# Optimization experiments

Hardware: AMD Instinct MI355X
Metric: run time of the kernel (lower is better)

## Reference

```python
import jax, jax.numpy as jnp
import numpy as np

N_CELL, N_TISSUE, H, NH = 200000, 2000, 256, 8
HD = H // NH
SCALE = HD ** -0.5
EPS = 1e-5


def _layernorm(x, g, b):
    m = jnp.mean(x, axis=-1, keepdims=True)
    v = jnp.mean((x - m) ** 2, axis=-1, keepdims=True)
    return (x - m) / jnp.sqrt(v + EPS) * g + b


def setup_inputs() -> dict:
    key = jax.random.key(0)
    ks = jax.random.split(key, 12)
    s = 0.02

    def lin(k):
        k1, k2 = jax.random.split(k)
        return (jax.random.normal(k1, (H, H), jnp.float32) * s,
                jax.random.normal(k2, (H,), jnp.float32) * s)

    Wq_bu, bq_bu = lin(ks[0])
    Wk_bu, bk_bu = lin(ks[1])
    Wv_bu, bv_bu = lin(ks[2])
    Wo_bu, bo_bu = lin(ks[3])
    Wv_td, bv_td = lin(ks[4])
    Wo_td, bo_td = lin(ks[5])
    return dict(
        cell_features=jax.random.normal(ks[6], (N_CELL, H), jnp.float32),
        tissue_features=jax.random.normal(ks[7], (N_TISSUE, H), jnp.float32),
        cluster_labels=jax.random.randint(ks[8], (N_CELL,), 0, N_TISSUE, dtype=jnp.int32),
        tissue_batch=jnp.zeros((N_TISSUE,), jnp.int32),
        Wq_bu=Wq_bu, bq_bu=bq_bu, Wk_bu=Wk_bu, bk_bu=bk_bu,
        Wv_bu=Wv_bu, bv_bu=bv_bu, Wo_bu=Wo_bu, bo_bu=bo_bu,
        Wv_td=Wv_td, bv_td=bv_td, Wo_td=Wo_td, bo_td=bo_td,
        ln_cell_g=jnp.ones((H,), jnp.float32), ln_cell_b=jnp.zeros((H,), jnp.float32),
        ln_tissue_g=jnp.ones((H,), jnp.float32), ln_tissue_b=jnp.zeros((H,), jnp.float32),
    )


def reference(cell_features, tissue_features, cluster_labels, tissue_batch,
              Wq_bu, bq_bu, Wk_bu, bk_bu, Wv_bu, bv_bu, Wo_bu, bo_bu,
              Wv_td, bv_td, Wo_td, bo_td,
              ln_cell_g, ln_cell_b, ln_tissue_g, ln_tissue_b):
    Nc = cell_features.shape[0]
    Nt = tissue_features.shape[0]

    # ---- bottom-up: each tissue node (1 query) attends over its cells (segment attention) ----
    Q = (tissue_features @ Wq_bu + bq_bu).reshape(Nt, NH, HD)   # [Nt, h, d]
    K = (cell_features @ Wk_bu + bk_bu).reshape(Nc, NH, HD)     # [Nc, h, d]
    V = (cell_features @ Wv_bu + bv_bu).reshape(Nc, NH, HD)     # [Nc, h, d]

    # per-cell score against its own cluster's tissue query
    scores = jnp.einsum('nhd,nhd->nh', K, Q[cluster_labels]) * SCALE  # [Nc, h]
    smax = jax.lax.stop_gradient(
        jax.ops.segment_max(scores, cluster_labels, num_segments=Nt))  # [Nt, h]
    ex = jnp.exp(scores - smax[cluster_labels])
    denom = jax.ops.segment_sum(ex, cluster_labels, num_segments=Nt)   # [Nt, h]
    w = ex / denom[cluster_labels]                                     # [Nc, h]
    attended = jax.ops.segment_sum(w[..., None] * V, cluster_labels,
                                   num_segments=Nt)                    # [Nt, h, d]
    attended = attended.reshape(Nt, H) @ Wo_bu + bo_bu

    counts = jax.ops.segment_sum(jnp.ones((Nc,), cell_features.dtype),
                                 cluster_labels, num_segments=Nt)
    tissue_updated = jnp.where(counts[:, None] > 0, attended, tissue_features)

    # ---- top-down: each cell attends to its single tissue token ----
    # softmax over a single key is identically 1, so q/k projections cancel:
    # attended_cell = out_proj(v_proj(tissue_updated[cluster]))
    td_per_tissue = (tissue_updated @ Wv_td + bv_td) @ Wo_td + bo_td   # [Nt, H]
    cell_updated = td_per_tissue[cluster_labels]                       # [Nc, H]

    cell_out = _layernorm(cell_features + cell_updated, ln_cell_g, ln_cell_b)
    tissue_out = _layernorm(tissue_features + tissue_updated, ln_tissue_g, ln_tissue_b)
    return (cell_out, tissue_out)
```

## Files before the change

### kernel.cpp

```cpp
#include <hip/hip_runtime.h>
#include <math.h>

#define NC 200000
#define NT 2000
#define HH 256
#define NH_ 8
#define SCALE 0.17677669529663687f
#define EPS 1e-5f


__global__ void k_hist(const int* __restrict__ labels, int* __restrict__ counts) {
  int i = blockIdx.x * 256 + threadIdx.x;
  if (i < NC) atomicAdd(&counts[labels[i]], 1);
}

__global__ void k_scan(const int* __restrict__ counts, int* __restrict__ offsets) {
  int tid = threadIdx.x;
  int base = tid * 32;
  int local[32];
  int s = 0;
  #pragma unroll
  for (int k = 0; k < 32; k++) {
    int idx = base + k;
    int v = (idx < NT) ? counts[idx] : 0;
    local[k] = s;
    s += v;
  }
  int incl = s;
  #pragma unroll
  for (int d = 1; d < 64; d <<= 1) {
    int o = __shfl_up(incl, d, 64);
    if (tid >= d) incl += o;
  }
  int excl = incl - s;
  #pragma unroll
  for (int k = 0; k < 32; k++) {
    int idx = base + k;
    if (idx < NT) offsets[idx] = excl + local[k];
  }
  if (tid == 63) offsets[NT] = incl;
}

__global__ void k_scatter(const int* __restrict__ labels, const int* __restrict__ offsets,
                          int* __restrict__ cursor, int* __restrict__ cindex) {
  int i = blockIdx.x * 256 + threadIdx.x;
  if (i < NC) {
    int c = labels[i];
    int pos = offsets[c] + atomicAdd(&cursor[c], 1);
    cindex[pos] = i;
  }
}


__global__ __launch_bounds__(256) void k_gemm_bias(
    const float* __restrict__ A, const float* __restrict__ W,
    const float* __restrict__ bias, float* __restrict__ C, int M)
{
  __shared__ float Al[16][33];
  __shared__ float Wl[32][HH];
  int tid = threadIdx.x;
  int r0 = blockIdx.x * 16;
  float acc[16];
  #pragma unroll
  for (int r = 0; r < 16; r++) acc[r] = 0.f;
  for (int k0 = 0; k0 < HH; k0 += 32) {
    for (int e = tid; e < 16 * 32; e += 256) {
      int r = e >> 5, k = e & 31;
      int row = r0 + r;
      Al[r][k] = (row < M) ? A[(size_t)row * HH + k0 + k] : 0.f;
    }
    for (int e = tid; e < 32 * HH; e += 256) {
      int k = e >> 8, j = e & 255;
      Wl[k][j] = W[(size_t)(k0 + k) * HH + j];
    }
    __syncthreads();
    for (int k = 0; k < 32; k++) {
      float w = Wl[k][tid];
      #pragma unroll
      for (int r = 0; r < 16; r++) acc[r] += Al[r][k] * w;
    }
    __syncthreads();
  }
  float bj = bias[tid];
  #pragma unroll
  for (int r = 0; r < 16; r++) {
    int row = r0 + r;
    if (row < M) C[(size_t)row * HH + tid] = acc[r] + bj;
  }
}


__global__ __launch_bounds__(256) void k_qproj(
    const float* __restrict__ Q, const float* __restrict__ Wk, float* __restrict__ Qproj)
{
  __shared__ float Al[64][33];
  __shared__ float Bl[32][257];
  int h = blockIdx.x & 7, tb = blockIdx.x >> 3;
  int t0 = tb * 64;
  int tid = threadIdx.x;
  for (int e = tid; e < 64 * 32; e += 256) {
    int r = e >> 5, d = e & 31;
    int t = t0 + r;
    Al[r][d] = (t < NT) ? Q[(size_t)t * HH + h * 32 + d] * SCALE : 0.f;
  }
  for (int e = tid; e < 256 * 32; e += 256) {
    int j = e >> 5, d = e & 31;
    Bl[d][j] = Wk[(size_t)j * HH + h * 32 + d];
  }
  __syncthreads();
  float acc[64];
  #pragma unroll
  for (int r = 0; r < 64; r++) acc[r] = 0.f;
  for (int d = 0; d < 32; d++) {
    float b = Bl[d][tid];
    #pragma unroll
    for (int r = 0; r < 64; r++) acc[r] += Al[r][d] * b;
  }
  for (int r = 0; r < 64; r++) {
    int t = t0 + r;
    if (t < NT) Qproj[((size_t)t * NH_ + h) * HH + tid] = acc[r];
  }
}

__global__ void k_bkq(const float* __restrict__ Q, const float* __restrict__ bk,
                      float* __restrict__ bkq) {
  int g = blockIdx.x * 256 + threadIdx.x;
  if (g < NT * NH_) {
    int t = g >> 3, h = g & 7;
    float s = 0.f;
    #pragma unroll
    for (int d = 0; d < 32; d++) s += bk[h * 32 + d] * Q[(size_t)t * HH + h * 32 + d];
    bkq[g] = s * SCALE;
  }
}


__global__ __launch_bounds__(256) void k_cellpass(
    const float* __restrict__ cell, const int* __restrict__ cindex,
    const int* __restrict__ offsets, const float* __restrict__ Qproj,
    const float* __restrict__ bkq, float* __restrict__ Cwn)
{
  int t = blockIdx.x;
  int n0 = offsets[t], n1 = offsets[t + 1];
  if (n1 == n0) return;
  int tid = threadIdx.x;
  int wave = tid >> 6, lane = tid & 63;

  float qp[NH_][4];
  #pragma unroll
  for (int h = 0; h < NH_; h++) {
    float4 v = *reinterpret_cast<const float4*>(&Qproj[((size_t)t * NH_ + h) * HH + lane * 4]);
    qp[h][0] = v.x; qp[h][1] = v.y; qp[h][2] = v.z; qp[h][3] = v.w;
  }
  float bq[NH_];
  #pragma unroll
  for (int h = 0; h < NH_; h++) bq[h] = bkq[t * NH_ + h];

  float m[NH_], dsum[NH_], cw[NH_][4];
  #pragma unroll
  for (int h = 0; h < NH_; h++) {
    m[h] = -1e30f; dsum[h] = 0.f;
    cw[h][0] = cw[h][1] = cw[h][2] = cw[h][3] = 0.f;
  }

  for (int i = n0 + wave; i < n1; i += 4) {
    int n = cindex[i];
    float4 x = *reinterpret_cast<const float4*>(&cell[(size_t)n * HH + lane * 4]);
    float p[NH_];
    #pragma unroll
    for (int h = 0; h < NH_; h++)
      p[h] = x.x * qp[h][0] + x.y * qp[h][1] + x.z * qp[h][2] + x.w * qp[h][3];
    #pragma unroll
    for (int d = 1; d < 64; d <<= 1) {
      #pragma unroll
      for (int h = 0; h < NH_; h++) p[h] += __shfl_xor(p[h], d, 64);
    }
    float s[NH_];
    bool need = false;
    #pragma unroll
    for (int h = 0; h < NH_; h++) { s[h] = p[h] + bq[h]; need = need || (s[h] > m[h]); }
    if (need) {
      #pragma unroll
      for (int h = 0; h < NH_; h++) {
        float mn = fmaxf(m[h], s[h]);
        float sc = __expf(m[h] - mn);
        m[h] = mn;
        dsum[h] *= sc;
        cw[h][0] *= sc; cw[h][1] *= sc; cw[h][2] *= sc; cw[h][3] *= sc;
      }
    }
    #pragma unroll
    for (int h = 0; h < NH_; h++) {
      float e = __expf(s[h] - m[h]);
      dsum[h] += e;
      cw[h][0] += e * x.x; cw[h][1] += e * x.y; cw[h][2] += e * x.z; cw[h][3] += e * x.w;
    }
  }

  __shared__ float mlds[4][NH_];
  __shared__ float dlds[4][NH_];
  __shared__ float cwlds[NH_][HH];
  if (lane == 0) {
    #pragma unroll
    for (int h = 0; h < NH_; h++) { mlds[wave][h] = m[h]; dlds[wave][h] = dsum[h]; }
  }
  __syncthreads();
  float sw[NH_], dtot[NH_];
  #pragma unroll
  for (int h = 0; h < NH_; h++) {
    float g = fmaxf(fmaxf(mlds[0][h], mlds[1][h]), fmaxf(mlds[2][h], mlds[3][h]));
    sw[h] = __expf(m[h] - g);
    dtot[h] = dlds[0][h] * __expf(mlds[0][h] - g) + dlds[1][h] * __expf(mlds[1][h] - g)
            + dlds[2][h] * __expf(mlds[2][h] - g) + dlds[3][h] * __expf(mlds[3][h] - g);
  }
  if (wave == 0) {
    #pragma unroll
    for (int h = 0; h < NH_; h++) {
      cwlds[h][lane * 4 + 0] = cw[h][0] * sw[h];
      cwlds[h][lane * 4 + 1] = cw[h][1] * sw[h];
      cwlds[h][lane * 4 + 2] = cw[h][2] * sw[h];
      cwlds[h][lane * 4 + 3] = cw[h][3] * sw[h];
    }
  }
  __syncthreads();
  #pragma unroll
  for (int w = 1; w < 4; w++) {
    if (wave == w) {
      #pragma unroll
      for (int h = 0; h < NH_; h++) {
        cwlds[h][lane * 4 + 0] += cw[h][0] * sw[h];
        cwlds[h][lane * 4 + 1] += cw[h][1] * sw[h];
        cwlds[h][lane * 4 + 2] += cw[h][2] * sw[h];
        cwlds[h][lane * 4 + 3] += cw[h][3] * sw[h];
      }
    }
    __syncthreads();
  }
  #pragma unroll
  for (int h = 0; h < NH_; h++)
    Cwn[((size_t)t * NH_ + h) * HH + tid] = cwlds[h][tid] / dtot[h];
}


#define TCH 8

__global__ __launch_bounds__(256) void k_tissuechain(
    const float* __restrict__ tissue, const int* __restrict__ counts,
    const float* __restrict__ Cwn,
    const float* __restrict__ Wv, const float* __restrict__ bv,
    const float* __restrict__ Wo, const float* __restrict__ bo,
    const float* __restrict__ Wvtd, const float* __restrict__ bvtd,
    const float* __restrict__ Wotd, const float* __restrict__ botd,
    const float* __restrict__ lng, const float* __restrict__ lnb,
    float* __restrict__ td, float* __restrict__ out_tissue)
{
  __shared__ float s_cwn[TCH][NH_ * HH];
  __shared__ float s_a[TCH][HH];
  __shared__ float s_tu[TCH][HH];
  __shared__ float s_tmp[TCH][HH];
  __shared__ float s_red[2][4];
  int t0 = blockIdx.x * TCH;
  int j = threadIdx.x;
  int h = j >> 5;

  for (int e = j; e < TCH * NH_ * HH; e += 256)
    ((float*)s_cwn)[e] = Cwn[(size_t)t0 * NH_ * HH + e];
  __syncthreads();

  float acc[TCH];
  #pragma unroll
  for (int t = 0; t < TCH; t++) acc[t] = 0.f;
  for (int k = 0; k < HH; k++) {
    float w = Wv[(size_t)k * HH + j];
    #pragma unroll
    for (int t = 0; t < TCH; t++) acc[t] += s_cwn[t][h * HH + k] * w;
  }
  {
    float bj = bv[j];
    #pragma unroll
    for (int t = 0; t < TCH; t++) s_a[t][j] = acc[t] + bj;
  }
  __syncthreads();

  #pragma unroll
  for (int t = 0; t < TCH; t++) acc[t] = 0.f;
  for (int k = 0; k < HH; k++) {
    float w = Wo[(size_t)k * HH + j];
    #pragma unroll
    for (int t = 0; t < TCH; t++) acc[t] += s_a[t][k] * w;
  }
  {
    float bj = bo[j];
    #pragma unroll
    for (int t = 0; t < TCH; t++) {
      int tt = t0 + t;
      s_tu[t][j] = (counts[tt] > 0) ? (acc[t] + bj) : tissue[(size_t)tt * HH + j];
    }
  }
  __syncthreads();

  #pragma unroll
  for (int t = 0; t < TCH; t++) acc[t] = 0.f;
  for (int k = 0; k < HH; k++) {
    float w = Wvtd[(size_t)k * HH + j];
    #pragma unroll
    for (int t = 0; t < TCH; t++) acc[t] += s_tu[t][k] * w;
  }
  {
    float bj = bvtd[j];
    #pragma unroll
    for (int t = 0; t < TCH; t++) s_tmp[t][j] = acc[t] + bj;
  }
  __syncthreads();

  #pragma unroll
  for (int t = 0; t < TCH; t++) acc[t] = 0.f;
  for (int k = 0; k < HH; k++) {
    float w = Wotd[(size_t)k * HH + j];
    #pragma unroll
    for (int t = 0; t < TCH; t++) acc[t] += s_tmp[t][k] * w;
  }
  {
    float bj = botd[j];
    #pragma unroll
    for (int t = 0; t < TCH; t++) td[(size_t)(t0 + t) * HH + j] = acc[t] + bj;
  }

  float gj = lng[j], bj2 = lnb[j];
  for (int t = 0; t < TCH; t++) {
    float y = tissue[(size_t)(t0 + t) * HH + j] + s_tu[t][j];
    float s1 = y, s2 = y * y;
    #pragma unroll
    for (int d = 1; d < 64; d <<= 1) { s1 += __shfl_xor(s1, d, 64); s2 += __shfl_xor(s2, d, 64); }
    int wv_ = j >> 6, ln_ = j & 63;
    __syncthreads();
    if (ln_ == 0) { s_red[0][wv_] = s1; s_red[1][wv_] = s2; }
    __syncthreads();
    s1 = s_red[0][0] + s_red[0][1] + s_red[0][2] + s_red[0][3];
    s2 = s_red[1][0] + s_red[1][1] + s_red[1][2] + s_red[1][3];
    float mean = s1 * (1.f / 256.f);
    float var = s2 * (1.f / 256.f) - mean * mean;
    float inv = rsqrtf(var + EPS);
    out_tissue[(size_t)(t0 + t) * HH + j] = (y - mean) * inv * gj + bj2;
  }
}


__global__ __launch_bounds__(256) void k_cellout(
    const float* __restrict__ cell, const float* __restrict__ td,
    const int* __restrict__ labels,
    const float* __restrict__ lng, const float* __restrict__ lnb,
    float* __restrict__ out)
{
  int row = blockIdx.x * 4 + (threadIdx.x >> 6);
  if (row >= NC) return;
  int lane = threadIdx.x & 63;
  int c = labels[row];
  float4 x = *reinterpret_cast<const float4*>(&cell[(size_t)row * HH + lane * 4]);
  float4 u = *reinterpret_cast<const float4*>(&td[(size_t)c * HH + lane * 4]);
  float y0 = x.x + u.x, y1 = x.y + u.y, y2 = x.z + u.z, y3 = x.w + u.w;
  float s1 = y0 + y1 + y2 + y3;
  float s2 = y0 * y0 + y1 * y1 + y2 * y2 + y3 * y3;
  #pragma unroll
  for (int d = 1; d < 64; d <<= 1) { s1 += __shfl_xor(s1, d, 64); s2 += __shfl_xor(s2, d, 64); }
  float mean = s1 * (1.f / 256.f);
  float var = s2 * (1.f / 256.f) - mean * mean;
  float inv = rsqrtf(var + EPS);
  float4 g = *reinterpret_cast<const float4*>(&lng[lane * 4]);
  float4 b = *reinterpret_cast<const float4*>(&lnb[lane * 4]);
  float4 o;
  o.x = (y0 - mean) * inv * g.x + b.x;
  o.y = (y1 - mean) * inv * g.y + b.y;
  o.z = (y2 - mean) * inv * g.z + b.z;
  o.w = (y3 - mean) * inv * g.w + b.w;
  *reinterpret_cast<float4*>(&out[(size_t)row * HH + lane * 4]) = o;
}


extern "C" void kernel_launch(void* const* d_in, const int* in_sizes, int n_in,
                              void* d_out, int out_size, void* d_ws, size_t ws_size,
                              hipStream_t stream) {
  const float* cell   = (const float*)d_in[0];
  const float* tissue = (const float*)d_in[1];
  const int*   labels = (const int*)d_in[2];
  const float* Wq = (const float*)d_in[4];  const float* bq = (const float*)d_in[5];
  const float* Wk = (const float*)d_in[6];  const float* bk = (const float*)d_in[7];
  const float* Wv = (const float*)d_in[8];  const float* bv = (const float*)d_in[9];
  const float* Wo = (const float*)d_in[10]; const float* bo = (const float*)d_in[11];
  const float* Wvtd = (const float*)d_in[12]; const float* bvtd = (const float*)d_in[13];
  const float* Wotd = (const float*)d_in[14]; const float* botd = (const float*)d_in[15];
  const float* lncg = (const float*)d_in[16]; const float* lncb = (const float*)d_in[17];
  const float* lntg = (const float*)d_in[18]; const float* lntb = (const float*)d_in[19];
  float* out_cell   = (float*)d_out;
  float* out_tissue = (float*)d_out + (size_t)NC * HH;

  char* w = (char*)d_ws;
  auto take = [&](size_t bytes) { void* p = (void*)w; w += (bytes + 255) & ~(size_t)255; return p; };
  int*   counts  = (int*)take((size_t)NT * 4);
  int*   cursor  = (int*)take((size_t)NT * 4);
  int*   offsets = (int*)take((size_t)(NT + 1) * 4);
  int*   cindex  = (int*)take((size_t)NC * 4);
  float* Q       = (float*)take((size_t)NT * HH * 4);
  float* Qproj   = (float*)take((size_t)NT * NH_ * HH * 4);
  float* bkq     = (float*)take((size_t)NT * NH_ * 4);
  float* Cwn     = (float*)take((size_t)NT * NH_ * HH * 4);
  float* td      = (float*)take((size_t)NT * HH * 4);

  hipMemsetAsync(counts, 0, 16384, stream);

  const int CB = (NC + 255) / 256;
  k_hist<<<CB, 256, 0, stream>>>(labels, counts);
  k_scan<<<1, 64, 0, stream>>>(counts, offsets);
  k_scatter<<<CB, 256, 0, stream>>>(labels, offsets, cursor, cindex);

  k_gemm_bias<<<(NT + 15) / 16, 256, 0, stream>>>(tissue, Wq, bq, Q, NT);
  k_qproj<<<8 * ((NT + 63) / 64), 256, 0, stream>>>(Q, Wk, Qproj);
  k_bkq<<<(NT * NH_ + 255) / 256, 256, 0, stream>>>(Q, bk, bkq);

  k_cellpass<<<NT, 256, 0, stream>>>(cell, cindex, offsets, Qproj, bkq, Cwn);

  k_tissuechain<<<NT / TCH, 256, 0, stream>>>(tissue, counts, Cwn,
      Wv, bv, Wo, bo, Wvtd, bvtd, Wotd, botd, lntg, lntb, td, out_tissue);

  k_cellout<<<NC / 4, 256, 0, stream>>>(cell, td, labels, lncg, lncb, out_cell);
}
```

Baseline: 479.5 us.

## Split cell segment softmax into score, exp, and weighted-sum passes with LDS score cache

Replaces the single-pass online-softmax cell kernel with a three-phase kernel. It computes all scores first, with 8 lanes per cell and two cells per sweep, and caches them as bf16 in LDS. It then computes the global max and exponentials, and finally accumulates the exp-weighted cell features without per-cell rescaling. This removes the full-wave shuffle reductions and rescale branches but reads cell features twice and stores scores and weights in bf16, which loses precision. Segments larger than SMAX=1024 cells are truncated, which risks wrong results for large clusters.

```diff
diff --git a/kernel.cpp b/kernel.cpp
--- a/kernel.cpp
+++ b/kernel.cpp
@@ -7,6 +7,7 @@
 #define NH_ 8
 #define SCALE 0.17677669529663687f
 #define EPS 1e-5f
+#define SMAX 1024
 
 
 __global__ void k_hist(const int* __restrict__ labels, int* __restrict__ counts) {
@@ -135,110 +136,179 @@
 }
 
 
-__global__ __launch_bounds__(256) void k_cellpass(
+__device__ inline unsigned pk2(float a, float b) {
+  unsigned ua = (__float_as_uint(a) + 0x8000u) >> 16;
+  unsigned ub = (__float_as_uint(b) + 0x8000u) & 0xFFFF0000u;
+  return ua | ub;
+}
+__device__ inline void unpk8(uint4 v, float* s) {
+  s[0] = __uint_as_float(v.x << 16); s[1] = __uint_as_float(v.x & 0xFFFF0000u);
+  s[2] = __uint_as_float(v.y << 16); s[3] = __uint_as_float(v.y & 0xFFFF0000u);
+  s[4] = __uint_as_float(v.z << 16); s[5] = __uint_as_float(v.z & 0xFFFF0000u);
+  s[6] = __uint_as_float(v.w << 16); s[7] = __uint_as_float(v.w & 0xFFFF0000u);
+}
+
+
+__global__ __launch_bounds__(256) void k_cellpass2(
     const float* __restrict__ cell, const int* __restrict__ cindex,
     const int* __restrict__ offsets, const float* __restrict__ Qproj,
     const float* __restrict__ bkq, float* __restrict__ Cwn)
 {
+  __shared__ float qp_lds[NH_][HH];
+  __shared__ uint4 slds[SMAX];
+  __shared__ float cwlds[NH_][HH];
+  __shared__ float red[4][NH_];
+
   int t = blockIdx.x;
   int n0 = offsets[t], n1 = offsets[t + 1];
-  if (n1 == n0) return;
+  int ncells = n1 - n0;
+  if (ncells <= 0) return;
+  if (ncells > SMAX) ncells = SMAX;
   int tid = threadIdx.x;
-  int wave = tid >> 6, lane = tid & 63;
-
-  float qp[NH_][4];
-  #pragma unroll
-  for (int h = 0; h < NH_; h++) {
-    float4 v = *reinterpret_cast<const float4*>(&Qproj[((size_t)t * NH_ + h) * HH + lane * 4]);
-    qp[h][0] = v.x; qp[h][1] = v.y; qp[h][2] = v.z; qp[h][3] = v.w;
-  }
+  int w = tid >> 6, lane = tid & 63;
+  int slot = lane >> 3, g = lane & 7;
+
+  for (int e = tid; e < NH_ * HH / 4; e += 256)
+    ((float4*)qp_lds)[e] = ((const float4*)(Qproj + (size_t)t * NH_ * HH))[e];
   float bq[NH_];
   #pragma unroll
   for (int h = 0; h < NH_; h++) bq[h] = bkq[t * NH_ + h];
-
-  float m[NH_], dsum[NH_], cw[NH_][4];
-  #pragma unroll
-  for (int h = 0; h < NH_; h++) {
-    m[h] = -1e30f; dsum[h] = 0.f;
-    cw[h][0] = cw[h][1] = cw[h][2] = cw[h][3] = 0.f;
-  }
-
-  for (int i = n0 + wave; i < n1; i += 4) {
-    int n = cindex[i];
+  __syncthreads();
+
+  float m[NH_];
+  #pragma unroll
+  for (int h = 0; h < NH_; h++) m[h] = -1e30f;
+
+  int nsweep = (ncells + 15) >> 4;
+  for (int j = w; j < nsweep; j += 4) {
+    int base = n0 + j * 16;
+    int ia = base + slot, ib = base + 8 + slot;
+    int na = cindex[min(ia, n1 - 1)];
+    int nb = cindex[min(ib, n1 - 1)];
+    float4 xa[8], xb[8];
+    #pragma unroll
+    for (int k = 0; k < 8; k++)
+      xa[k] = *reinterpret_cast<const float4*>(&cell[(size_t)na * HH + g * 4 + 32 * k]);
+    #pragma unroll
+    for (int k = 0; k < 8; k++)
+      xb[k] = *reinterpret_cast<const float4*>(&cell[(size_t)nb * HH + g * 4 + 32 * k]);
+
+    float pa[NH_], pb[NH_];
+    #pragma unroll
+    for (int h = 0; h < NH_; h++) { pa[h] = 0.f; pb[h] = 0.f; }
+    #pragma unroll
+    for (int h = 0; h < NH_; h++) {
+      #pragma unroll
+      for (int k = 0; k < 8; k++) {
+        float4 q = *reinterpret_cast<const float4*>(&qp_lds[h][g * 4 + 32 * k]);
+        pa[h] += xa[k].x * q.x + xa[k].y * q.y + xa[k].z * q.z + xa[k].w * q.w;
+        pb[h] += xb[k].x * q.x + xb[k].y * q.y + xb[k].z * q.z + xb[k].w * q.w;
+      }
+    }
+    #pragma unroll
+    for (int d = 1; d < 8; d <<= 1) {
+      #pragma unroll
+      for (int h = 0; h < NH_; h++) {
+        pa[h] += __shfl_xor(pa[h], d, 64);
+        pb[h] += __shfl_xor(pb[h], d, 64);
+      }
+    }
+    #pragma unroll
+    for (int h = 0; h < NH_; h++) { pa[h] += bq[h]; pb[h] += bq[h]; }
+    bool va = ia < n1, vb = ib < n1;
+    if (va) {
+      #pragma unroll
+      for (int h = 0; h < NH_; h++) m[h] = fmaxf(m[h], pa[h]);
+    }
+    if (vb) {
+      #pragma unroll
+      for (int h = 0; h < NH_; h++) m[h] = fmaxf(m[h], pb[h]);
+    }
+    if (g == 0) {
+      if (va) slds[ia - n0] = make_uint4(pk2(pa[0], pa[1]), pk2(pa[2], pa[3]),
+                                         pk2(pa[4], pa[5]), pk2(pa[6], pa[7]));
+      if (vb) slds[ib - n0] = make_uint4(pk2(pb[0], pb[1]), pk2(pb[2], pb[3]),
+                                         pk2(pb[4], pb[5]), pk2(pb[6], pb[7]));
+    }
+  }
+
+  #pragma unroll
+  for (int d = 8; d < 64; d <<= 1) {
+    #pragma unroll
+    for (int h = 0; h < NH_; h++) m[h] = fmaxf(m[h], __shfl_xor(m[h], d, 64));
+  }
+  if (lane == 0) {
+    #pragma unroll
+    for (int h = 0; h < NH_; h++) red[w][h] = m[h];
+  }
+  __syncthreads();
+  #pragma unroll
+  for (int h = 0; h < NH_; h++)
+    m[h] = fmaxf(fmaxf(red[0][h], red[1][h]), fmaxf(red[2][h], red[3][h]));
+  __syncthreads();
+
+  float dsum[NH_];
+  #pragma unroll
+  for (int h = 0; h < NH_; h++) dsum[h] = 0.f;
+  for (int i = tid; i < ncells; i += 256) {
+    uint4 sv = slds[i];
+    float s[NH_], e[NH_];
+    unpk8(sv, s);
+    #pragma unroll
+    for (int h = 0; h < NH_; h++) { e[h] = __expf(s[h] - m[h]); dsum[h] += e[h]; }
+    slds[i] = make_uint4(pk2(e[0], e[1]), pk2(e[2], e[3]), pk2(e[4], e[5]), pk2(e[6], e[7]));
+  }
+  #pragma unroll
+  for (int d = 1; d < 64; d <<= 1) {
+    #pragma unroll
+    for (int h = 0; h < NH_; h++) dsum[h] += __shfl_xor(dsum[h], d, 64);
+  }
+  if (lane == 0) {
+    #pragma unroll
+    for (int h = 0; h < NH_; h++) red[w][h] = dsum[h];
+  }
+  __syncthreads();
+  float dinv[NH_];
+  #pragma unroll
+  for (int h = 0; h < NH_; h++)
+    dinv[h] = 1.f / (red[0][h] + red[1][h] + red[2][h] + red[3][h]);
+
+  float cw[NH_][4];
+  #pragma unroll
+  for (int h = 0; h < NH_; h++) { cw[h][0] = cw[h][1] = cw[h][2] = cw[h][3] = 0.f; }
+  for (int i = w; i < ncells; i += 4) {
+    int n = cindex[n0 + i];
     float4 x = *reinterpret_cast<const float4*>(&cell[(size_t)n * HH + lane * 4]);
-    float p[NH_];
+    float e[NH_];
+    unpk8(slds[i], e);
+    #pragma unroll
+    for (int h = 0; h < NH_; h++) {
+      cw[h][0] += e[h] * x.x; cw[h][1] += e[h] * x.y;
+      cw[h][2] += e[h] * x.z; cw[h][3] += e[h] * x.w;
+    }
+  }
+  if (w == 0) {
     #pragma unroll
     for (int h = 0; h < NH_; h++)
-      p[h] = x.x * qp[h][0] + x.y * qp[h][1] + x.z * qp[h][2] + x.w * qp[h][3];
-    #pragma unroll
-    for (int d = 1; d < 64; d <<= 1) {
-      #pragma unroll
-      for (int h = 0; h < NH_; h++) p[h] += __shfl_xor(p[h], d, 64);
-    }
-    float s[NH_];
-    bool need = false;
-    #pragma unroll
-    for (int h = 0; h < NH_; h++) { s[h] = p[h] + bq[h]; need = need || (s[h] > m[h]); }
-    if (need) {
+      *reinterpret_cast<float4*>(&cwlds[h][lane * 4]) =
+          make_float4(cw[h][0], cw[h][1], cw[h][2], cw[h][3]);
+  }
+  __syncthreads();
+  #pragma unroll
+  for (int ww = 1; ww < 4; ww++) {
+    if (w == ww) {
       #pragma unroll
       for (int h = 0; h < NH_; h++) {
-        float mn = fmaxf(m[h], s[h]);
-        float sc = __expf(m[h] - mn);
-        m[h] = mn;
-        dsum[h] *= sc;
-        cw[h][0] *= sc; cw[h][1] *= sc; cw[h][2] *= sc; cw[h][3] *= sc;
+        float4 c = *reinterpret_cast<float4*>(&cwlds[h][lane * 4]);
+        c.x += cw[h][0]; c.y += cw[h][1]; c.z += cw[h][2]; c.w += cw[h][3];
+        *reinterpret_cast<float4*>(&cwlds[h][lane * 4]) = c;
       }
     }
-    #pragma unroll
-    for (int h = 0; h < NH_; h++) {
-      float e = __expf(s[h] - m[h]);
-      dsum[h] += e;
-      cw[h][0] += e * x.x; cw[h][1] += e * x.y; cw[h][2] += e * x.z; cw[h][3] += e * x.w;
-    }
-  }
-
-  __shared__ float mlds[4][NH_];
-  __shared__ float dlds[4][NH_];
-  __shared__ float cwlds[NH_][HH];
-  if (lane == 0) {
-    #pragma unroll
-    for (int h = 0; h < NH_; h++) { mlds[wave][h] = m[h]; dlds[wave][h] = dsum[h]; }
-  }
-  __syncthreads();
-  float sw[NH_], dtot[NH_];
-  #pragma unroll
-  for (int h = 0; h < NH_; h++) {
-    float g = fmaxf(fmaxf(mlds[0][h], mlds[1][h]), fmaxf(mlds[2][h], mlds[3][h]));
-    sw[h] = __expf(m[h] - g);
-    dtot[h] = dlds[0][h] * __expf(mlds[0][h] - g) + dlds[1][h] * __expf(mlds[1][h] - g)
-            + dlds[2][h] * __expf(mlds[2][h] - g) + dlds[3][h] * __expf(mlds[3][h] - g);
-  }
-  if (wave == 0) {
-    #pragma unroll
-    for (int h = 0; h < NH_; h++) {
-      cwlds[h][lane * 4 + 0] = cw[h][0] * sw[h];
-      cwlds[h][lane * 4 + 1] = cw[h][1] * sw[h];
-      cwlds[h][lane * 4 + 2] = cw[h][2] * sw[h];
-      cwlds[h][lane * 4 + 3] = cw[h][3] * sw[h];
-    }
-  }
-  __syncthreads();
-  #pragma unroll
-  for (int w = 1; w < 4; w++) {
-    if (wave == w) {
-      #pragma unroll
-      for (int h = 0; h < NH_; h++) {
-        cwlds[h][lane * 4 + 0] += cw[h][0] * sw[h];
-        cwlds[h][lane * 4 + 1] += cw[h][1] * sw[h];
-        cwlds[h][lane * 4 + 2] += cw[h][2] * sw[h];
-        cwlds[h][lane * 4 + 3] += cw[h][3] * sw[h];
-      }
-    }
     __syncthreads();
   }
   #pragma unroll
   for (int h = 0; h < NH_; h++)
-    Cwn[((size_t)t * NH_ + h) * HH + tid] = cwlds[h][tid] / dtot[h];
+    Cwn[((size_t)t * NH_ + h) * HH + tid] = cwlds[h][tid] * dinv[h];
 }
 
 
@@ -417,7 +487,7 @@
   k_qproj<<<8 * ((NT + 63) / 64), 256, 0, stream>>>(Q, Wk, Qproj);
   k_bkq<<<(NT * NH_ + 255) / 256, 256, 0, stream>>>(Q, bk, bkq);
 
-  k_cellpass<<<NT, 256, 0, stream>>>(cell, cindex, offsets, Qproj, bkq, Cwn);
+  k_cellpass2<<<NT, 256, 0, stream>>>(cell, cindex, offsets, Qproj, bkq, Cwn);
 
   k_tissuechain<<<NT / TCH, 256, 0, stream>>>(tissue, counts, Cwn,
       Wv, bv, Wo, bo, Wvtd, bvtd, Wotd, botd, lntg, lntb, td, out_tissue);
```

New measurement: 487.6 us. Within noise of the previous version (+1.7%).
